# Kernel optimization log

Hardware: AMD Instinct MI355X
Metric: run time of the kernel (lower is better)

Reference implementation:

```python
import jax, jax.numpy as jnp
import numpy as np

BS, C, T = 8, 4096, 512          # batch, channels/tokens, flattened spatial (= q_dim)
H, HD = 8, 64                     # n_heads, head_dim = output_dim // n_heads
OUT_DIM = 512
SCALE = float(np.sqrt(OUT_DIM))   # module uses sqrt(output_dim), not sqrt(head_dim)


def setup_inputs() -> dict:
    key = jax.random.key(0)
    ks = jax.random.split(key, 7)
    init = 0.02
    return {
        "q": jax.random.normal(ks[0], (BS, C, T), jnp.float32),
        "k": jax.random.normal(ks[1], (BS, C, T), jnp.float32),
        "v": jax.random.normal(ks[2], (BS, C, T), jnp.float32),
        # per-head Linear weights, torch layout (out, in) stacked over heads
        "Wq": jax.random.normal(ks[3], (H, HD, T), jnp.float32) * init,
        "Wk": jax.random.normal(ks[4], (H, HD, T), jnp.float32) * init,
        "Wv": jax.random.normal(ks[5], (H, HD, T), jnp.float32) * init,
        "Wo": jax.random.normal(ks[6], (OUT_DIM, H * HD), jnp.float32) * init,
    }


def reference(q, k, v, Wq, Wk, Wv, Wo):
    bs, c, t = q.shape
    # batched per-head projections: (b, C, T) x (H, HD, T) -> (b, H, C, HD)
    qh = jnp.einsum("bct,hdt->bhcd", q, Wq)
    kh = jnp.einsum("bct,hdt->bhcd", k, Wk)
    vh = jnp.einsum("bct,hdt->bhcd", v, Wv)
    # attention contracts over the channel axis c (faithful to 'bct,bcs->bts')
    scores = jnp.einsum("bhcd,bhce->bhde", qh, kh) / SCALE  # (b, H, HD, HD)
    w = jax.nn.softmax(scores, axis=-1)
    # 'bts,bcs->bct' per head -> (b, H, C, HD)
    attn = jnp.einsum("bhde,bhce->bhcd", w, vh)
    # concat heads along last dim: (b, C, H*HD)
    cat = attn.transpose(0, 2, 1, 3).reshape(bs, c, H * HD)
    out = cat @ Wo.T  # (b, C, OUT_DIM); dropout p=0 -> identity
    return out.reshape(bs, -1, t)  # view(bs, -1, *spatial)
```

## Files before the change

kernel.cpp:

```cpp
#include <hip/hip_runtime.h>

#define BS    8
#define CDIM  4096
#define TDIM  512
#define NH    8
#define HD    64
#define NDIM  512
#define INV_SCALE 0.044194173824159216f

typedef __bf16 bf16x8 __attribute__((ext_vector_type(8)));
typedef float  f32x4  __attribute__((ext_vector_type(4)));

static __device__ __forceinline__ unsigned short f2b(float f) {
    union { float f; unsigned int i; } x; x.f = f;
    unsigned int r = x.i + 0x7FFFu + ((x.i >> 16) & 1u);
    return (unsigned short)(r >> 16);
}

static __device__ __forceinline__ void gl2lds16(const unsigned short* g,
                                                unsigned short* l) {
    __builtin_amdgcn_global_load_lds(
        (const __attribute__((address_space(1))) void*)g,
        (__attribute__((address_space(3))) void*)l, 16, 0, 0);
}

__global__ __launch_bounds__(256) void transpose_qk_kernel(
    const float* __restrict__ q, const float* __restrict__ k,
    unsigned short* __restrict__ qT, unsigned short* __restrict__ kT)
{
    __shared__ unsigned short Ls[64 * 65];

    const int z = blockIdx.z;
    const int b = z & 7;
    const float* src = (z >> 3) ? k : q;
    unsigned short* dst = (z >> 3) ? kT : qT;

    const int c0 = blockIdx.x * 64;
    const int t0 = blockIdx.y * 64;
    const int tid = threadIdx.x;

    {
        const int r = tid >> 2, seg = (tid & 3) * 16;
        const float* p = src + ((size_t)b * CDIM + c0 + r) * TDIM + t0 + seg;
        float4 f0 = *(const float4*)p, f1 = *(const float4*)(p + 4);
        float4 f2 = *(const float4*)(p + 8), f3 = *(const float4*)(p + 12);
        float ff[16] = {f0.x, f0.y, f0.z, f0.w, f1.x, f1.y, f1.z, f1.w,
                        f2.x, f2.y, f2.z, f2.w, f3.x, f3.y, f3.z, f3.w};
#pragma unroll
        for (int j = 0; j < 16; j++) Ls[(seg + j) * 65 + r] = f2b(ff[j]);
    }
    __syncthreads();
    {
        const int tp = tid >> 2, cs = (tid & 3) * 16;
        alignas(16) unsigned short u[16];
#pragma unroll
        for (int j = 0; j < 16; j++) u[j] = Ls[tp * 65 + cs + j];
        unsigned short* o = dst + ((size_t)b * TDIM + t0 + tp) * CDIM + c0 + cs;
        *(float4*)o = *(const float4*)u;
        *(float4*)(o + 8) = *(const float4*)(u + 8);
    }
}

__global__ __launch_bounds__(256) void cvt_kernel(
    const float* __restrict__ in, unsigned short* __restrict__ out, int n8)
{
    int i = blockIdx.x * 256 + threadIdx.x;
    if (i >= n8) return;
    float4 f0 = ((const float4*)in)[i * 2], f1 = ((const float4*)in)[i * 2 + 1];
    alignas(16) unsigned short t[8] = {f2b(f0.x), f2b(f0.y), f2b(f0.z), f2b(f0.w),
                                       f2b(f1.x), f2b(f1.y), f2b(f1.z), f2b(f1.w)};
    ((float4*)out)[i] = *(const float4*)t;
}

__global__ __launch_bounds__(256) void gemm128_kernel(
    const void* __restrict__ Av, int a_f32, size_t sAb,
    const unsigned short* __restrict__ B, size_t sBb,
    void* __restrict__ Cv, int c_f32, int writeT, int ldc, size_t sCb,
    int ldk, int K, int zshift, int zmask, size_t sCsplit)
{
    __shared__ unsigned short As[128 * 32];
    __shared__ unsigned short Bs[128 * 32];

    const int tid  = threadIdx.x;
    const int wave = tid >> 6, lane = tid & 63;
    const int quad = lane >> 4, l16 = lane & 15;
    const int wm = wave >> 1, wn = wave & 1;
    const int m0 = blockIdx.x * 128, n0 = blockIdx.y * 128;
    const int z = blockIdx.z;
    const int b = z >> zshift;
    const int ks = z & zmask;
    const int kbase = ks * K;

    const unsigned short* Bb = B + (size_t)b * sBb;

    f32x4 acc[4][4];
#pragma unroll
    for (int i = 0; i < 4; i++)
#pragma unroll
        for (int j = 0; j < 4; j++) acc[i][j] = (f32x4){0.f, 0.f, 0.f, 0.f};

    const int ldr = lane >> 2, ldc8 = (lane & 3) * 8;
    const int ar = tid >> 1, as0 = (tid & 1) * 16;

    for (int k0 = kbase; k0 < kbase + K; k0 += 32) {
        __syncthreads();
        if (a_f32) {
            const float* Ab = (const float*)Av + (size_t)b * sAb +
                              (size_t)(m0 + ar) * ldk + k0 + as0;
            float4 f0 = *(const float4*)Ab,       f1 = *(const float4*)(Ab + 4);
            float4 f2 = *(const float4*)(Ab + 8), f3 = *(const float4*)(Ab + 12);
            alignas(16) unsigned short t16[16] = {
                f2b(f0.x), f2b(f0.y), f2b(f0.z), f2b(f0.w),
                f2b(f1.x), f2b(f1.y), f2b(f1.z), f2b(f1.w),
                f2b(f2.x), f2b(f2.y), f2b(f2.z), f2b(f2.w),
                f2b(f3.x), f2b(f3.y), f2b(f3.z), f2b(f3.w)};
            *(float4*)&As[ar * 32 + as0]     = ((const float4*)t16)[0];
            *(float4*)&As[ar * 32 + as0 + 8] = ((const float4*)t16)[1];
        } else {
            const unsigned short* Ab = (const unsigned short*)Av + (size_t)b * sAb;
#pragma unroll
            for (int i = 0; i < 2; i++) {
                int panel = wave * 2 + i;
                gl2lds16(&Ab[(size_t)(m0 + panel * 16 + ldr) * ldk + k0 + ldc8],
                         &As[panel * 512]);
            }
        }
#pragma unroll
        for (int i = 0; i < 2; i++) {
            int panel = wave * 2 + i;
            gl2lds16(&Bb[(size_t)(n0 + panel * 16 + ldr) * ldk + k0 + ldc8],
                     &Bs[panel * 512]);
        }
        __syncthreads();

        bf16x8 af[4], bf[4];
#pragma unroll
        for (int i = 0; i < 4; i++) {
            af[i] = *(const bf16x8*)&As[(wm * 64 + i * 16 + l16) * 32 + quad * 8];
            bf[i] = *(const bf16x8*)&Bs[(wn * 64 + i * 16 + l16) * 32 + quad * 8];
        }
#pragma unroll
        for (int mb = 0; mb < 4; mb++)
#pragma unroll
            for (int nb = 0; nb < 4; nb++)
                acc[mb][nb] = __builtin_amdgcn_mfma_f32_16x16x32_bf16(
                    af[mb], bf[nb], acc[mb][nb], 0, 0, 0);
    }

    const size_t offC = (size_t)b * sCb + (size_t)ks * sCsplit;
#pragma unroll
    for (int mb = 0; mb < 4; mb++)
#pragma unroll
        for (int nb = 0; nb < 4; nb++)
#pragma unroll
            for (int r = 0; r < 4; r++) {
                int row = m0 + wm * 64 + mb * 16 + quad * 4 + r;
                int col = n0 + wn * 64 + nb * 16 + l16;
                size_t idx = offC + (writeT ? (size_t)col * ldc + row
                                            : (size_t)row * ldc + col);
                if (c_f32) ((float*)Cv)[idx] = acc[mb][nb][r];
                else ((unsigned short*)Cv)[idx] = f2b(acc[mb][nb][r]);
            }
}

__global__ __launch_bounds__(256) void reduceG_kernel(
    const float* __restrict__ P, unsigned short* __restrict__ G)
{
    const int i = blockIdx.x * 256 + threadIdx.x;
    const float4* p = (const float4*)P + (size_t)i * 2;
    const size_t st = 2097152 / 4;
    float4 a0 = p[0], a1 = p[1];
#pragma unroll
    for (int s = 1; s < 4; s++) {
        float4 b0 = p[(size_t)s * st], b1 = p[(size_t)s * st + 1];
        a0.x += b0.x; a0.y += b0.y; a0.z += b0.z; a0.w += b0.w;
        a1.x += b1.x; a1.y += b1.y; a1.z += b1.z; a1.w += b1.w;
    }
    alignas(16) unsigned short t[8] = {f2b(a0.x), f2b(a0.y), f2b(a0.z), f2b(a0.w),
                                       f2b(a1.x), f2b(a1.y), f2b(a1.z), f2b(a1.w)};
    ((float4*)G)[i] = *(const float4*)t;
}

__global__ __launch_bounds__(256) void gemm64_kernel(
    const void* __restrict__ Av, int a_f32, size_t sAb, size_t sAh,
    const unsigned short* __restrict__ B, size_t sBb, size_t sBh,
    void* __restrict__ Cv, int c_f32, int writeT, int ldc, size_t sCb, size_t sCh,
    int K, int hshift, int hmask)
{
    __shared__ unsigned short As[64][40];
    __shared__ unsigned short Bs[64][40];

    const int tid  = threadIdx.x;
    const int wave = tid >> 6, lane = tid & 63;
    const int quad = lane >> 4, l16 = lane & 15;
    const int m0 = blockIdx.x * 64, n0 = blockIdx.y * 64;
    const int bz = blockIdx.z;
    const int b = bz >> hshift, h = bz & hmask;

    f32x4 acc[4];
#pragma unroll
    for (int i = 0; i < 4; i++) acc[i] = (f32x4){0.f, 0.f, 0.f, 0.f};

    const int ldrow = tid >> 2, ldseg = (tid & 3) * 8;
    const size_t offA = (size_t)b * sAb + (size_t)h * sAh;
    const size_t offB = (size_t)b * sBb + (size_t)h * sBh;

    for (int k0 = 0; k0 < K; k0 += 32) {
        __syncthreads();
        if (a_f32) {
            const float* p = (const float*)Av + offA + (size_t)(m0 + ldrow) * K + k0 + ldseg;
            float4 lo = *(const float4*)p, hi = *(const float4*)(p + 4);
            alignas(16) unsigned short t8[8] = {
                f2b(lo.x), f2b(lo.y), f2b(lo.z), f2b(lo.w),
                f2b(hi.x), f2b(hi.y), f2b(hi.z), f2b(hi.w)};
            *(float4*)&As[ldrow][ldseg] = *(const float4*)t8;
        } else {
            const unsigned short* p = (const unsigned short*)Av + offA +
                                      (size_t)(m0 + ldrow) * K + k0 + ldseg;
            *(float4*)&As[ldrow][ldseg] = *(const float4*)p;
        }
        {
            const unsigned short* p = B + offB + (size_t)(n0 + ldrow) * K + k0 + ldseg;
            *(float4*)&Bs[ldrow][ldseg] = *(const float4*)p;
        }
        __syncthreads();

        bf16x8 a = *(const bf16x8*)&As[wave * 16 + l16][quad * 8];
#pragma unroll
        for (int nb = 0; nb < 4; nb++) {
            bf16x8 bb = *(const bf16x8*)&Bs[nb * 16 + l16][quad * 8];
            acc[nb] = __builtin_amdgcn_mfma_f32_16x16x32_bf16(a, bb, acc[nb], 0, 0, 0);
        }
    }

    const size_t offC = (size_t)b * sCb + (size_t)h * sCh;
#pragma unroll
    for (int nb = 0; nb < 4; nb++)
#pragma unroll
        for (int r = 0; r < 4; r++) {
            int row = m0 + wave * 16 + quad * 4 + r;
            int col = n0 + nb * 16 + l16;
            size_t idx = offC + (writeT ? (size_t)col * ldc + row
                                        : (size_t)row * ldc + col);
            if (c_f32) ((float*)Cv)[idx] = acc[nb][r];
            else ((unsigned short*)Cv)[idx] = f2b(acc[nb][r]);
        }
}

__global__ __launch_bounds__(256) void transpose_wv_kernel(
    const float* __restrict__ Wv, unsigned short* __restrict__ WvT)
{
    int i = blockIdx.x * 256 + threadIdx.x;
    int h = i >> 15, r = i & 32767;
    int t = r >> 6, e = i & 63;
    WvT[i] = f2b(Wv[(size_t)h * 32768 + (size_t)e * 512 + t]);
}

__global__ __launch_bounds__(64) void softmax_kernel(
    const float* __restrict__ S, unsigned short* __restrict__ w)
{
    const int bh = blockIdx.x;
    const int d  = threadIdx.x;
    const float* s = S + (size_t)bh * (HD * HD) + d * HD;
    float v[64];
    float m = -1e30f;
#pragma unroll
    for (int e = 0; e < 64; e++) { v[e] = s[e] * INV_SCALE; m = fmaxf(m, v[e]); }
    float sum = 0.f;
#pragma unroll
    for (int e = 0; e < 64; e++) { v[e] = __expf(v[e] - m); sum += v[e]; }
    float rinv = 1.0f / sum;
    unsigned short* o = w + (size_t)bh * (HD * HD) + d * HD;
#pragma unroll
    for (int e = 0; e < 64; e++) o[e] = f2b(v[e] * rinv);
}

extern "C" void kernel_launch(void* const* d_in, const int* in_sizes, int n_in,
                              void* d_out, int out_size, void* d_ws, size_t ws_size,
                              hipStream_t stream)
{
    const float* q  = (const float*)d_in[0];
    const float* k  = (const float*)d_in[1];
    const float* v  = (const float*)d_in[2];
    const float* Wq = (const float*)d_in[3];
    const float* Wk = (const float*)d_in[4];
    const float* Wv = (const float*)d_in[5];
    const float* Wo = (const float*)d_in[6];

    unsigned short* qT   = (unsigned short*)d_ws;
    unsigned short* kT   = qT + 16777216;
    unsigned short* G    = kT + 16777216;
    unsigned short* tmpT = G + 2097152;
    unsigned short* WkB  = tmpT + 2097152;
    unsigned short* WoB  = WkB + 262144;
    unsigned short* WvT  = WoB + 262144;
    unsigned short* w    = WvT + 262144;
    unsigned short* WveT = w + 262144;
    unsigned short* W2   = WveT + 2097152;
    float*          S    = (float*)(W2 + 2097152);
    float*          P    = (float*)tmpT;

    transpose_qk_kernel<<<dim3(64, 8, 16), 256, 0, stream>>>(q, k, qT, kT);

    gemm128_kernel<<<dim3(4, 4, BS * 4), 256, 0, stream>>>(
        qT, 0, 16777216 / 8, kT, 2097152,
        P, 1, 0, 512, 262144, 4096, 1024, 2, 3, 2097152);
    reduceG_kernel<<<1024, 256, 0, stream>>>(P, G);

    cvt_kernel<<<128, 256, 0, stream>>>(Wk, WkB, 32768);
    cvt_kernel<<<128, 256, 0, stream>>>(Wo, WoB, 32768);
    transpose_wv_kernel<<<1024, 256, 0, stream>>>(Wv, WvT);

    gemm128_kernel<<<dim3(4, 4, BS), 256, 0, stream>>>(
        G, 0, 262144, WkB, 0,
        tmpT, 0, 1, 512, 262144, 512, 512, 0, 0, 0);

    gemm64_kernel<<<dim3(1, 1, 64), 256, 0, stream>>>(
        Wq, 1, 0, 32768, tmpT, 262144, 32768,
        S, 1, 0, 64, 32768, 4096, 512, 3, 7);

    softmax_kernel<<<64, 64, 0, stream>>>(S, w);

    gemm64_kernel<<<dim3(1, 8, 64), 256, 0, stream>>>(
        w, 0, 32768, 4096, WvT, 0, 32768,
        WveT, 0, 1, 512, 262144, 64, 64, 3, 7);

    gemm128_kernel<<<dim3(4, 4, BS), 256, 0, stream>>>(
        WoB, 0, 0, WveT, 262144,
        W2, 0, 0, 512, 262144, 512, 512, 0, 0, 0);

    gemm128_kernel<<<dim3(32, 4, BS), 256, 0, stream>>>(
        v, 1, 2097152, W2, 262144,
        d_out, 1, 0, 512, 2097152, 512, 512, 0, 0, 0);
}
```

Before: 385.0 us.

## Double-buffer LDS tiles in gemm128 to overlap global loads with MFMA

```diff
diff --git a/kernel.cpp b/kernel.cpp
--- a/kernel.cpp
+++ b/kernel.cpp
@@ -24,6 +24,12 @@
         (__attribute__((address_space(3))) void*)l, 16, 0, 0);
 }
 
+#define PIPE_BARRIER() do {                                          \
+    asm volatile("s_waitcnt vmcnt(0) lgkmcnt(0)" ::: "memory");      \
+    __builtin_amdgcn_s_barrier();                                    \
+    asm volatile("" ::: "memory");                                   \
+} while (0)
+
 __global__ __launch_bounds__(256) void transpose_qk_kernel(
     const float* __restrict__ q, const float* __restrict__ k,
     unsigned short* __restrict__ qT, unsigned short* __restrict__ kT)
@@ -78,8 +84,8 @@
     void* __restrict__ Cv, int c_f32, int writeT, int ldc, size_t sCb,
     int ldk, int K, int zshift, int zmask, size_t sCsplit)
 {
-    __shared__ unsigned short As[128 * 32];
-    __shared__ unsigned short Bs[128 * 32];
+    __shared__ unsigned short As[2][128 * 32];
+    __shared__ unsigned short Bs[2][128 * 32];
 
     const int tid  = threadIdx.x;
     const int wave = tid >> 6, lane = tid & 63;
@@ -91,7 +97,9 @@
     const int ks = z & zmask;
     const int kbase = ks * K;
 
-    const unsigned short* Bb = B + (size_t)b * sBb;
+    const unsigned short* Bb   = B + (size_t)b * sBb;
+    const unsigned short* Ab16 = (const unsigned short*)Av + (size_t)b * sAb;
+    const float*          Ab32 = (const float*)Av + (size_t)b * sAb;
 
     f32x4 acc[4][4];
 #pragma unroll
@@ -102,49 +110,85 @@
     const int ldr = lane >> 2, ldc8 = (lane & 3) * 8;
     const int ar = tid >> 1, as0 = (tid & 1) * 16;
 
-    for (int k0 = kbase; k0 < kbase + K; k0 += 32) {
-        __syncthreads();
-        if (a_f32) {
-            const float* Ab = (const float*)Av + (size_t)b * sAb +
-                              (size_t)(m0 + ar) * ldk + k0 + as0;
-            float4 f0 = *(const float4*)Ab,       f1 = *(const float4*)(Ab + 4);
-            float4 f2 = *(const float4*)(Ab + 8), f3 = *(const float4*)(Ab + 12);
+    const int nt = K / 32;
+
+    if (a_f32) {
+        const float* p = Ab32 + (size_t)(m0 + ar) * ldk + kbase + as0;
+        float4 f0 = *(const float4*)p,       f1 = *(const float4*)(p + 4);
+        float4 f2 = *(const float4*)(p + 8), f3 = *(const float4*)(p + 12);
+        alignas(16) unsigned short t16[16] = {
+            f2b(f0.x), f2b(f0.y), f2b(f0.z), f2b(f0.w),
+            f2b(f1.x), f2b(f1.y), f2b(f1.z), f2b(f1.w),
+            f2b(f2.x), f2b(f2.y), f2b(f2.z), f2b(f2.w),
+            f2b(f3.x), f2b(f3.y), f2b(f3.z), f2b(f3.w)};
+        *(float4*)&As[0][ar * 32 + as0]     = ((const float4*)t16)[0];
+        *(float4*)&As[0][ar * 32 + as0 + 8] = ((const float4*)t16)[1];
+    } else {
+#pragma unroll
+        for (int i = 0; i < 2; i++) {
+            int panel = wave * 2 + i;
+            gl2lds16(&Ab16[(size_t)(m0 + panel * 16 + ldr) * ldk + kbase + ldc8],
+                     &As[0][panel * 512]);
+        }
+    }
+#pragma unroll
+    for (int i = 0; i < 2; i++) {
+        int panel = wave * 2 + i;
+        gl2lds16(&Bb[(size_t)(n0 + panel * 16 + ldr) * ldk + kbase + ldc8],
+                 &Bs[0][panel * 512]);
+    }
+    PIPE_BARRIER();
+
+    for (int t = 0; t < nt; ++t) {
+        const int cur = t & 1, nxt = cur ^ 1;
+        const int kn = kbase + (t + 1) * 32;
+        const bool pf = (t + 1 < nt);
+
+        float4 f0, f1, f2, f3;
+        if (pf) {
+            if (a_f32) {
+                const float* p = Ab32 + (size_t)(m0 + ar) * ldk + kn + as0;
+                f0 = *(const float4*)p;       f1 = *(const float4*)(p + 4);
+                f2 = *(const float4*)(p + 8); f3 = *(const float4*)(p + 12);
+            } else {
+#pragma unroll
+                for (int i = 0; i < 2; i++) {
+                    int panel = wave * 2 + i;
+                    gl2lds16(&Ab16[(size_t)(m0 + panel * 16 + ldr) * ldk + kn + ldc8],
+                             &As[nxt][panel * 512]);
+                }
+            }
+#pragma unroll
+            for (int i = 0; i < 2; i++) {
+                int panel = wave * 2 + i;
+                gl2lds16(&Bb[(size_t)(n0 + panel * 16 + ldr) * ldk + kn + ldc8],
+                         &Bs[nxt][panel * 512]);
+            }
+        }
+
+        bf16x8 af[4], bf[4];
+#pragma unroll
+        for (int i = 0; i < 4; i++) {
+            af[i] = *(const bf16x8*)&As[cur][(wm * 64 + i * 16 + l16) * 32 + quad * 8];
+            bf[i] = *(const bf16x8*)&Bs[cur][(wn * 64 + i * 16 + l16) * 32 + quad * 8];
+        }
+#pragma unroll
+        for (int mb = 0; mb < 4; mb++)
+#pragma unroll
+            for (int nb = 0; nb < 4; nb++)
+                acc[mb][nb] = __builtin_amdgcn_mfma_f32_16x16x32_bf16(
+                    af[mb], bf[nb], acc[mb][nb], 0, 0, 0);
+
+        if (pf && a_f32) {
             alignas(16) unsigned short t16[16] = {
                 f2b(f0.x), f2b(f0.y), f2b(f0.z), f2b(f0.w),
                 f2b(f1.x), f2b(f1.y), f2b(f1.z), f2b(f1.w),
                 f2b(f2.x), f2b(f2.y), f2b(f2.z), f2b(f2.w),
                 f2b(f3.x), f2b(f3.y), f2b(f3.z), f2b(f3.w)};
-            *(float4*)&As[ar * 32 + as0]     = ((const float4*)t16)[0];
-            *(float4*)&As[ar * 32 + as0 + 8] = ((const float4*)t16)[1];
-        } else {
-            const unsigned short* Ab = (const unsigned short*)Av + (size_t)b * sAb;
-#pragma unroll
-            for (int i = 0; i < 2; i++) {
-                int panel = wave * 2 + i;
-                gl2lds16(&Ab[(size_t)(m0 + panel * 16 + ldr) * ldk + k0 + ldc8],
-                         &As[panel * 512]);
-            }
-        }
-#pragma unroll
-        for (int i = 0; i < 2; i++) {
-            int panel = wave * 2 + i;
-            gl2lds16(&Bb[(size_t)(n0 + panel * 16 + ldr) * ldk + k0 + ldc8],
-                     &Bs[panel * 512]);
-        }
-        __syncthreads();
-
-        bf16x8 af[4], bf[4];
-#pragma unroll
-        for (int i = 0; i < 4; i++) {
-            af[i] = *(const bf16x8*)&As[(wm * 64 + i * 16 + l16) * 32 + quad * 8];
-            bf[i] = *(const bf16x8*)&Bs[(wn * 64 + i * 16 + l16) * 32 + quad * 8];
-        }
-#pragma unroll
-        for (int mb = 0; mb < 4; mb++)
-#pragma unroll
-            for (int nb = 0; nb < 4; nb++)
-                acc[mb][nb] = __builtin_amdgcn_mfma_f32_16x16x32_bf16(
-                    af[mb], bf[nb], acc[mb][nb], 0, 0, 0);
+            *(float4*)&As[nxt][ar * 32 + as0]     = ((const float4*)t16)[0];
+            *(float4*)&As[nxt][ar * 32 + as0 + 8] = ((const float4*)t16)[1];
+        }
+        PIPE_BARRIER();
     }
 
     const size_t offC = (size_t)b * sCb + (size_t)ks * sCsplit;
```

Measured after the change: 383.1 us. No clear change (-0.5%).

## Pipeline gemm128 with multi-stage async LDS loads, swizzle, and split-K small GEMMs

Applied to the files above, without the earlier changes.

```diff
diff --git a/kernel.cpp b/kernel.cpp
--- a/kernel.cpp
+++ b/kernel.cpp
@@ -73,13 +73,13 @@
 }
 
 __global__ __launch_bounds__(256) void gemm128_kernel(
-    const void* __restrict__ Av, int a_f32, size_t sAb,
+    const unsigned short* __restrict__ A, size_t sAb,
     const unsigned short* __restrict__ B, size_t sBb,
     void* __restrict__ Cv, int c_f32, int writeT, int ldc, size_t sCb,
     int ldk, int K, int zshift, int zmask, size_t sCsplit)
 {
-    __shared__ unsigned short As[128 * 32];
-    __shared__ unsigned short Bs[128 * 32];
+    __shared__ unsigned short As[5][128 * 32];
+    __shared__ unsigned short Bs[5][128 * 32];
 
     const int tid  = threadIdx.x;
     const int wave = tid >> 6, lane = tid & 63;
@@ -87,10 +87,10 @@
     const int wm = wave >> 1, wn = wave & 1;
     const int m0 = blockIdx.x * 128, n0 = blockIdx.y * 128;
     const int z = blockIdx.z;
-    const int b = z >> zshift;
-    const int ks = z & zmask;
+    const int b = z >> zshift, ks = z & zmask;
     const int kbase = ks * K;
 
+    const unsigned short* Ab = A + (size_t)b * sAb;
     const unsigned short* Bb = B + (size_t)b * sBb;
 
     f32x4 acc[4][4];
@@ -99,45 +99,49 @@
 #pragma unroll
         for (int j = 0; j < 4; j++) acc[i][j] = (f32x4){0.f, 0.f, 0.f, 0.f};
 
-    const int ldr = lane >> 2, ldc8 = (lane & 3) * 8;
-    const int ar = tid >> 1, as0 = (tid & 1) * 16;
-
-    for (int k0 = kbase; k0 < kbase + K; k0 += 32) {
-        __syncthreads();
-        if (a_f32) {
-            const float* Ab = (const float*)Av + (size_t)b * sAb +
-                              (size_t)(m0 + ar) * ldk + k0 + as0;
-            float4 f0 = *(const float4*)Ab,       f1 = *(const float4*)(Ab + 4);
-            float4 f2 = *(const float4*)(Ab + 8), f3 = *(const float4*)(Ab + 12);
-            alignas(16) unsigned short t16[16] = {
-                f2b(f0.x), f2b(f0.y), f2b(f0.z), f2b(f0.w),
-                f2b(f1.x), f2b(f1.y), f2b(f1.z), f2b(f1.w),
-                f2b(f2.x), f2b(f2.y), f2b(f2.z), f2b(f2.w),
-                f2b(f3.x), f2b(f3.y), f2b(f3.z), f2b(f3.w)};
-            *(float4*)&As[ar * 32 + as0]     = ((const float4*)t16)[0];
-            *(float4*)&As[ar * 32 + as0 + 8] = ((const float4*)t16)[1];
-        } else {
-            const unsigned short* Ab = (const unsigned short*)Av + (size_t)b * sAb;
-#pragma unroll
-            for (int i = 0; i < 2; i++) {
-                int panel = wave * 2 + i;
-                gl2lds16(&Ab[(size_t)(m0 + panel * 16 + ldr) * ldk + k0 + ldc8],
-                         &As[panel * 512]);
-            }
-        }
+    const int ldr  = lane >> 2;
+    const int fr_w = (ldr & 3) ^ ((ldr >> 2) & 1);
+    const int gcol = ((lane & 3) ^ fr_w) * 8;
+    const int fr_r = (l16 & 3) ^ ((l16 >> 2) & 1);
+    const int qsw  = (quad ^ fr_r) * 8;
+
+    const int nt = K / 32;
+
+    auto stage = [&](int t) {
+        const int kk = kbase + t * 32;
+        unsigned short* as = &As[t % 5][0];
+        unsigned short* bs = &Bs[t % 5][0];
 #pragma unroll
         for (int i = 0; i < 2; i++) {
-            int panel = wave * 2 + i;
-            gl2lds16(&Bb[(size_t)(n0 + panel * 16 + ldr) * ldk + k0 + ldc8],
-                     &Bs[panel * 512]);
-        }
-        __syncthreads();
-
+            const int panel = wave * 2 + i;
+            gl2lds16(&Ab[(size_t)(m0 + panel * 16 + ldr) * ldk + kk + gcol],
+                     &as[panel * 512]);
+            gl2lds16(&Bb[(size_t)(n0 + panel * 16 + ldr) * ldk + kk + gcol],
+                     &bs[panel * 512]);
+        }
+    };
+
+    stage(0);
+    if (nt > 1) stage(1);
+    if (nt > 2) stage(2);
+
+    for (int t = 0; t < nt; ++t) {
+        if (t + 3 < nt) stage(t + 3);
+        const int ahead = nt - 1 - t;
+        if (ahead >= 3)      asm volatile("s_waitcnt vmcnt(12)" ::: "memory");
+        else if (ahead == 2) asm volatile("s_waitcnt vmcnt(8)"  ::: "memory");
+        else if (ahead == 1) asm volatile("s_waitcnt vmcnt(4)"  ::: "memory");
+        else                 asm volatile("s_waitcnt vmcnt(0)"  ::: "memory");
+        __builtin_amdgcn_s_barrier();
+        asm volatile("" ::: "memory");
+
+        const unsigned short* as = &As[t % 5][0];
+        const unsigned short* bs = &Bs[t % 5][0];
         bf16x8 af[4], bf[4];
 #pragma unroll
         for (int i = 0; i < 4; i++) {
-            af[i] = *(const bf16x8*)&As[(wm * 64 + i * 16 + l16) * 32 + quad * 8];
-            bf[i] = *(const bf16x8*)&Bs[(wn * 64 + i * 16 + l16) * 32 + quad * 8];
+            af[i] = *(const bf16x8*)&as[(wm * 64 + i * 16 + l16) * 32 + qsw];
+            bf[i] = *(const bf16x8*)&bs[(wn * 64 + i * 16 + l16) * 32 + qsw];
         }
 #pragma unroll
         for (int mb = 0; mb < 4; mb++)
@@ -298,22 +302,28 @@
     unsigned short* WveT = w + 262144;
     unsigned short* W2   = WveT + 2097152;
     float*          S    = (float*)(W2 + 2097152);
-    float*          P    = (float*)tmpT;
+    float*          P1   = (float*)tmpT;
+    unsigned short* vB   = qT;
+    float*          PK   = (float*)kT;
 
     transpose_qk_kernel<<<dim3(64, 8, 16), 256, 0, stream>>>(q, k, qT, kT);
 
     gemm128_kernel<<<dim3(4, 4, BS * 4), 256, 0, stream>>>(
-        qT, 0, 16777216 / 8, kT, 2097152,
-        P, 1, 0, 512, 262144, 4096, 1024, 2, 3, 2097152);
-    reduceG_kernel<<<1024, 256, 0, stream>>>(P, G);
+        qT, 2097152, kT, 2097152,
+        P1, 1, 0, 512, 262144, 4096, 1024, 2, 3, 2097152);
+
+    cvt_kernel<<<8192, 256, 0, stream>>>(v, vB, 2097152);
+
+    reduceG_kernel<<<1024, 256, 0, stream>>>(P1, G);
 
     cvt_kernel<<<128, 256, 0, stream>>>(Wk, WkB, 32768);
     cvt_kernel<<<128, 256, 0, stream>>>(Wo, WoB, 32768);
     transpose_wv_kernel<<<1024, 256, 0, stream>>>(Wv, WvT);
 
-    gemm128_kernel<<<dim3(4, 4, BS), 256, 0, stream>>>(
-        G, 0, 262144, WkB, 0,
-        tmpT, 0, 1, 512, 262144, 512, 512, 0, 0, 0);
+    gemm128_kernel<<<dim3(4, 4, BS * 4), 256, 0, stream>>>(
+        G, 262144, WkB, 0,
+        PK, 1, 1, 512, 262144, 512, 128, 2, 3, 2097152);
+    reduceG_kernel<<<1024, 256, 0, stream>>>(PK, tmpT);
 
     gemm64_kernel<<<dim3(1, 1, 64), 256, 0, stream>>>(
         Wq, 1, 0, 32768, tmpT, 262144, 32768,
@@ -325,11 +335,12 @@
         w, 0, 32768, 4096, WvT, 0, 32768,
         WveT, 0, 1, 512, 262144, 64, 64, 3, 7);
 
-    gemm128_kernel<<<dim3(4, 4, BS), 256, 0, stream>>>(
-        WoB, 0, 0, WveT, 262144,
-        W2, 0, 0, 512, 262144, 512, 512, 0, 0, 0);
+    gemm128_kernel<<<dim3(4, 4, BS * 4), 256, 0, stream>>>(
+        WoB, 0, WveT, 262144,
+        PK, 1, 0, 512, 262144, 512, 128, 2, 3, 2097152);
+    reduceG_kernel<<<1024, 256, 0, stream>>>(PK, W2);
 
     gemm128_kernel<<<dim3(32, 4, BS), 256, 0, stream>>>(
-        v, 1, 2097152, W2, 262144,
+        vB, 2097152, W2, 262144,
         d_out, 1, 0, 512, 2097152, 512, 512, 0, 0, 0);
 }
```

Result: no change. 385.1 us (+0.0%).
